# Kernel tuning notes

Measured on AMD Instinct MI355X. Metric: run time of the kernel, lower is better.

## Reference

```python
import jax, jax.numpy as jnp
import numpy as np

N_NODES = 5000
N_EDGES = 160000
HID = 64
NODE_F = 4
TASK_F = 4
BATCH = 512


def _glorot(key, shape):
    fan_in = shape[-1]
    return jax.random.normal(key, shape, dtype=jnp.float32) / jnp.sqrt(jnp.float32(fan_in))


def setup_inputs() -> dict:
    key = jax.random.key(0)
    ks = jax.random.split(key, 16)
    x = jax.random.normal(ks[0], (N_NODES, NODE_F), dtype=jnp.float32)
    edge_index = jax.random.randint(ks[1], (2, N_EDGES), 0, N_NODES, dtype=jnp.int64)
    task_feat = jax.random.normal(ks[2], (BATCH, TASK_F), dtype=jnp.float32)
    return {
        "x": x,
        "edge_index": edge_index,
        "task_feat": task_feat,
        # SAGEConv layer 1: out = lin_l(mean_neigh) + lin_r(x); lin_l has bias, lin_r (root) has no bias (PyG default)
        "Wl1": _glorot(ks[3], (HID, NODE_F)), "bl1": jnp.zeros((HID,), jnp.float32),
        "Wr1": _glorot(ks[4], (HID, NODE_F)),
        # SAGEConv layer 2
        "Wl2": _glorot(ks[5], (HID, HID)), "bl2": jnp.zeros((HID,), jnp.float32),
        "Wr2": _glorot(ks[6], (HID, HID)),
        # task_encoder: Linear(4,64) -> ReLU -> Linear(64,64)
        "Wt1": _glorot(ks[7], (HID, TASK_F)), "bt1": jnp.zeros((HID,), jnp.float32),
        "Wt2": _glorot(ks[8], (HID, HID)), "bt2": jnp.zeros((HID,), jnp.float32),
        # classifier: Linear(128,64) -> ReLU -> Linear(64,1)
        "Wc1": _glorot(ks[9], (HID, 2 * HID)), "bc1": jnp.zeros((HID,), jnp.float32),
        "Wc2": _glorot(ks[10], (1, HID)), "bc2": jnp.zeros((1,), jnp.float32),
    }


def _sage_conv(x, src, dst, Wl, bl, Wr):
    # PyG SAGEConv(mean): messages flow src -> dst; mean over incoming neighbors
    msg_sum = jax.ops.segment_sum(x[src], dst, num_segments=N_NODES)
    deg = jax.ops.segment_sum(jnp.ones((src.shape[0],), x.dtype), dst, num_segments=N_NODES)
    mean_neigh = msg_sum / jnp.maximum(deg, 1.0)[:, None]
    return mean_neigh @ Wl.T + bl + x @ Wr.T


def reference(x, edge_index, task_feat,
              Wl1, bl1, Wr1, Wl2, bl2, Wr2,
              Wt1, bt1, Wt2, bt2, Wc1, bc1, Wc2, bc2):
    src, dst = edge_index[0], edge_index[1]
    h = jax.nn.relu(_sage_conv(x, src, dst, Wl1, bl1, Wr1))        # [N, HID]
    h = jax.nn.relu(_sage_conv(h, src, dst, Wl2, bl2, Wr2))        # [N, HID]
    t = jax.nn.relu(task_feat @ Wt1.T + bt1) @ Wt2.T + bt2         # [B, HID]
    # classifier on concat([h, t]) == split Wc1 into h-part and t-part; avoids materializing the concat
    h_part = h @ Wc1[:, :HID].T                                    # [N, HID]
    t_part = t @ Wc1[:, HID:].T + bc1                              # [B, HID]
    hidden = jax.nn.relu(h_part[None, :, :] + t_part[:, None, :])  # [B, N, HID]
    scores = jnp.einsum('bnh,h->bn', hidden, Wc2[0]) + bc2[0]      # [B, N]
    return scores
```

## Files before the change

kernel.cpp:

```cpp
#include <hip/hip_runtime.h>

#define N_NODES 5000
#define N_EDGES 160000
#define HID 64
#define BATCH 512
#define NSL 64
#define EPS (N_EDGES / NSL)
#define SLOTS 12
#define NROW (NSL * SLOTS)
#define CSTRIDE 96


__global__ __launch_bounds__(256) void sort_kernel(
        const int* __restrict__ ei, const float* __restrict__ task_feat,
        const float* __restrict__ Wt1, const float* __restrict__ bt1,
        const float* __restrict__ Wt2, const float* __restrict__ bt2,
        const float* __restrict__ Wc1, const float* __restrict__ bc1,
        const float* __restrict__ Wl1, const float* __restrict__ Wr1,
        const float* __restrict__ Wl2, const float* __restrict__ Wr2,
        int* __restrict__ slots, int* __restrict__ cnt, float* __restrict__ t_part,
        float* __restrict__ Wl1T, float* __restrict__ Wr1T,
        float* __restrict__ Wl2T, float* __restrict__ Wr2T,
        float* __restrict__ Wc1hT) {
    int tid = threadIdx.x;
    int blk = blockIdx.x;
    __shared__ union SM {
        int cur[N_NODES];
        struct { float s1[4][64]; float s2[4][64]; } t;
    } sm;

    if (blk < NSL) {
        int s = blk;
        for (int i = tid; i < N_NODES; i += 256) sm.cur[i] = 0;
        __syncthreads();
        int base = s * EPS;
        for (int j = tid; j < EPS; j += 256) {
            int src = ei[base + j];
            int dst = ei[N_EDGES + base + j];
            int q = atomicAdd(&sm.cur[dst], 1);
            if (q < SLOTS) slots[dst * NROW + s * SLOTS + q] = src;
        }
        __syncthreads();
        for (int n = tid; n < N_NODES; n += 256)
            cnt[s * N_NODES + n] = min(sm.cur[n], SLOTS);
    } else if (blk < NSL + 4) {
        int w = blk - NSL;
        if (w == 0) {
            for (int idx = tid; idx < 4096; idx += 256) {
                int k = idx >> 6, h = idx & 63;
                Wl2T[idx] = Wl2[h * 64 + k];
            }
        } else if (w == 1) {
            for (int idx = tid; idx < 4096; idx += 256) {
                int k = idx >> 6, h = idx & 63;
                Wr2T[idx] = Wr2[h * 64 + k];
            }
        } else if (w == 2) {
            for (int idx = tid; idx < 4096; idx += 256) {
                int k = idx >> 6, h = idx & 63;
                Wc1hT[idx] = Wc1[h * 128 + k];
            }
        } else {
            int k = tid >> 6, h = tid & 63;
            Wl1T[tid] = Wl1[h * 4 + k];
            Wr1T[tid] = Wr1[h * 4 + k];
        }
    } else {
        int grp = tid >> 6, h = tid & 63;
        int b = (blk - (NSL + 4)) * 4 + grp;
        float4 tf = ((const float4*)task_feat)[b];
        float4 w1 = ((const float4*)Wt1)[h];
        float v = bt1[h] + tf.x * w1.x + tf.y * w1.y + tf.z * w1.z + tf.w * w1.w;
        sm.t.s1[grp][h] = fmaxf(v, 0.f);
        __syncthreads();
        const float4* w2r = (const float4*)(Wt2 + h * 64);
        const float4* s1v = (const float4*)sm.t.s1[grp];
        float v2 = bt2[h];
#pragma unroll
        for (int q = 0; q < 16; q++) {
            float4 w = w2r[q]; float4 ss = s1v[q];
            v2 += ss.x * w.x + ss.y * w.y + ss.z * w.z + ss.w * w.w;
        }
        sm.t.s2[grp][h] = v2;
        __syncthreads();
        const float4* wcr = (const float4*)(Wc1 + h * 128 + 64);
        const float4* s2v = (const float4*)sm.t.s2[grp];
        float p = bc1[h];
#pragma unroll
        for (int q = 0; q < 16; q++) {
            float4 w = wcr[q]; float4 ss = s2v[q];
            p += ss.x * w.x + ss.y * w.y + ss.z * w.z + ss.w * w.w;
        }
        t_part[b * 64 + h] = p;
    }
}

__global__ __launch_bounds__(256) void layer1_kernel(
        const float* __restrict__ x, const int* __restrict__ slots,
        const int* __restrict__ cnt,
        const float* __restrict__ Wl1T, const float* __restrict__ bl1,
        const float* __restrict__ Wr1T,
        int* __restrict__ deg, int* __restrict__ compact, float* __restrict__ h1) {
    int lane = threadIdx.x & 63, grp = threadIdx.x >> 6;
    int n = blockIdx.x * 4 + grp;
    int c = cnt[lane * N_NODES + n];
    int scan = c;
#pragma unroll
    for (int off = 1; off < 64; off <<= 1) {
        int nb = __shfl_up(scan, off);
        if (lane >= off) scan += nb;
    }
    int d = __shfl(scan, 63);
    int excl = scan - c;
    const int* chunk = slots + n * NROW + lane * SLOTS;
    float4 xs = make_float4(0.f, 0.f, 0.f, 0.f);
    for (int q = 0; q < c; q++) {
        int src = chunk[q];
        float4 xv = ((const float4*)x)[src];
        xs.x += xv.x; xs.y += xv.y; xs.z += xv.z; xs.w += xv.w;
        int pos = excl + q;
        if (pos < CSTRIDE) compact[n * CSTRIDE + pos] = src;
    }
#pragma unroll
    for (int off = 1; off < 64; off <<= 1) {
        xs.x += __shfl_xor(xs.x, off);
        xs.y += __shfl_xor(xs.y, off);
        xs.z += __shfl_xor(xs.z, off);
        xs.w += __shfl_xor(xs.w, off);
    }
    if (d > CSTRIDE) d = CSTRIDE;
    if (lane == 0) deg[n] = d;
    float inv = 1.f / fmaxf((float)d, 1.f);
    float m0 = xs.x * inv, m1 = xs.y * inv, m2 = xs.z * inv, m3 = xs.w * inv;
    float4 xn = ((const float4*)x)[n];
    float v = bl1[lane]
            + m0 * Wl1T[lane] + m1 * Wl1T[64 + lane]
            + m2 * Wl1T[128 + lane] + m3 * Wl1T[192 + lane]
            + xn.x * Wr1T[lane] + xn.y * Wr1T[64 + lane]
            + xn.z * Wr1T[128 + lane] + xn.w * Wr1T[192 + lane];
    h1[n * 64 + lane] = fmaxf(v, 0.f);
}

__global__ __launch_bounds__(256) void layer2_kernel(
        const float* __restrict__ h1, const int* __restrict__ deg,
        const int* __restrict__ compact,
        const float* __restrict__ Wl2T, const float* __restrict__ bl2,
        const float* __restrict__ Wr2T, const float* __restrict__ Wc1hT,
        float* __restrict__ h_part) {
    int h = threadIdx.x & 63, grp = threadIdx.x >> 6;
    int n = blockIdx.x * 4 + grp;
    int d = deg[n];
    const int* bucket = compact + n * CSTRIDE;
    float a0 = 0.f, a1 = 0.f, a2 = 0.f, a3 = 0.f;
    int j = 0;
    for (; j + 4 <= d; j += 4) {
        int e0 = bucket[j], e1 = bucket[j + 1], e2 = bucket[j + 2], e3 = bucket[j + 3];
        a0 += h1[e0 * 64 + h];
        a1 += h1[e1 * 64 + h];
        a2 += h1[e2 * 64 + h];
        a3 += h1[e3 * 64 + h];
    }
    for (; j < d; j++) a0 += h1[bucket[j] * 64 + h];
    float m = (a0 + a1 + a2 + a3) / fmaxf((float)d, 1.f);

    __shared__ float shm[4][64], shh[4][64], shh2[4][64];
    shm[grp][h] = m;
    shh[grp][h] = h1[n * 64 + h];
    __syncthreads();
    float v = bl2[h];
#pragma unroll
    for (int k = 0; k < 64; k++)
        v += shm[grp][k] * Wl2T[k * 64 + h] + shh[grp][k] * Wr2T[k * 64 + h];
    shh2[grp][h] = fmaxf(v, 0.f);
    __syncthreads();
    float p = 0.f;
#pragma unroll
    for (int k = 0; k < 64; k++) p += shh2[grp][k] * Wc1hT[k * 64 + h];
    h_part[n * 64 + h] = p;
}

__global__ __launch_bounds__(256) void scores_kernel(
        const float* __restrict__ h_part, const float* __restrict__ t_part,
        const float* __restrict__ Wc2, const float* __restrict__ bc2,
        float* __restrict__ out) {
    int tid = threadIdx.x;
    int n = blockIdx.x * 256 + tid;
    bool valid = n < N_NODES;
    int nn = valid ? n : (N_NODES - 1);
    float hr[64];
    const float4* hp = (const float4*)(h_part + nn * 64);
#pragma unroll
    for (int i = 0; i < 16; i++) {
        float4 v = hp[i];
        hr[4 * i + 0] = v.x; hr[4 * i + 1] = v.y;
        hr[4 * i + 2] = v.z; hr[4 * i + 3] = v.w;
    }
    float b2 = bc2[0];
    int b0 = blockIdx.y * 8;
    for (int bb = 0; bb < 8; bb++) {
        const float* tp = t_part + (b0 + bb) * 64;
        float acc = 0.f;
#pragma unroll
        for (int h = 0; h < 64; h++)
            acc = fmaf(fmaxf(hr[h] + tp[h], 0.f), Wc2[h], acc);
        if (valid) out[(b0 + bb) * N_NODES + n] = acc + b2;
    }
}

extern "C" void kernel_launch(void* const* d_in, const int* in_sizes, int n_in,
                              void* d_out, int out_size, void* d_ws, size_t ws_size,
                              hipStream_t stream) {
    const float* x    = (const float*)d_in[0];
    const int*   ei   = (const int*)d_in[1];
    const float* task = (const float*)d_in[2];
    const float* Wl1  = (const float*)d_in[3];
    const float* bl1  = (const float*)d_in[4];
    const float* Wr1  = (const float*)d_in[5];
    const float* Wl2  = (const float*)d_in[6];
    const float* bl2  = (const float*)d_in[7];
    const float* Wr2  = (const float*)d_in[8];
    const float* Wt1  = (const float*)d_in[9];
    const float* bt1  = (const float*)d_in[10];
    const float* Wt2  = (const float*)d_in[11];
    const float* bt2  = (const float*)d_in[12];
    const float* Wc1  = (const float*)d_in[13];
    const float* bc1  = (const float*)d_in[14];
    const float* Wc2  = (const float*)d_in[15];
    const float* bc2  = (const float*)d_in[16];
    float* out = (float*)d_out;

    char* ws = (char*)d_ws;
    int*   slots   = (int*)(ws + 0);
    int*   cnt     = (int*)(ws + 15360000);
    int*   compact = (int*)(ws + 16640000);
    int*   deg     = (int*)(ws + 18560000);
    float* h1      = (float*)(ws + 18580000);
    float* h_part  = (float*)(ws + 19860000);
    float* t_part  = (float*)(ws + 21140000);
    float* Wl1T  = (float*)(ws + 21271072);
    float* Wr1T  = (float*)(ws + 21272096);
    float* Wl2T  = (float*)(ws + 21273120);
    float* Wr2T  = (float*)(ws + 21289504);
    float* Wc1hT = (float*)(ws + 21305888);

    sort_kernel<<<NSL + 4 + BATCH / 4, 256, 0, stream>>>(
        ei, task, Wt1, bt1, Wt2, bt2, Wc1, bc1, Wl1, Wr1, Wl2, Wr2,
        slots, cnt, t_part, Wl1T, Wr1T, Wl2T, Wr2T, Wc1hT);
    layer1_kernel<<<N_NODES / 4, 256, 0, stream>>>(x, slots, cnt, Wl1T, bl1, Wr1T,
                                                   deg, compact, h1);
    layer2_kernel<<<N_NODES / 4, 256, 0, stream>>>(h1, deg, compact, Wl2T, bl2, Wr2T,
                                                   Wc1hT, h_part);
    scores_kernel<<<dim3(20, 64), 256, 0, stream>>>(h_part, t_part, Wc2, bc2, out);
}
```

Baseline: 148.1 us.

## Drop weight transpose pass, stage weights in LDS, reslice slot layout

Removes the global weight-transpose blocks from the sort kernel. Layer2 now loads the raw row-major weights into padded LDS tiles in every block and reads them with float4 dot products, and layer1 reads the original weight rows as float4. The slot buffer is reorganised per slice (slice-major, node, slot) so each sort block writes a contiguous region, and the scores kernel processes 16 batches per block instead of 8. The trade-off is that every layer2 block reloads about 48KB of weights into LDS, which lowers occupancy and repeats global reads.

```diff
diff --git a/kernel.cpp b/kernel.cpp
--- a/kernel.cpp
+++ b/kernel.cpp
@@ -7,7 +7,6 @@
 #define NSL 64
 #define EPS (N_EDGES / NSL)
 #define SLOTS 12
-#define NROW (NSL * SLOTS)
 #define CSTRIDE 96
 
 
@@ -16,12 +15,7 @@
         const float* __restrict__ Wt1, const float* __restrict__ bt1,
         const float* __restrict__ Wt2, const float* __restrict__ bt2,
         const float* __restrict__ Wc1, const float* __restrict__ bc1,
-        const float* __restrict__ Wl1, const float* __restrict__ Wr1,
-        const float* __restrict__ Wl2, const float* __restrict__ Wr2,
-        int* __restrict__ slots, int* __restrict__ cnt, float* __restrict__ t_part,
-        float* __restrict__ Wl1T, float* __restrict__ Wr1T,
-        float* __restrict__ Wl2T, float* __restrict__ Wr2T,
-        float* __restrict__ Wc1hT) {
+        int* __restrict__ slots, int* __restrict__ cnt, float* __restrict__ t_part) {
     int tid = threadIdx.x;
     int blk = blockIdx.x;
     __shared__ union SM {
@@ -34,40 +28,19 @@
         for (int i = tid; i < N_NODES; i += 256) sm.cur[i] = 0;
         __syncthreads();
         int base = s * EPS;
+        int* myslots = slots + s * (N_NODES * SLOTS);
         for (int j = tid; j < EPS; j += 256) {
             int src = ei[base + j];
             int dst = ei[N_EDGES + base + j];
             int q = atomicAdd(&sm.cur[dst], 1);
-            if (q < SLOTS) slots[dst * NROW + s * SLOTS + q] = src;
+            if (q < SLOTS) myslots[dst * SLOTS + q] = src;
         }
         __syncthreads();
         for (int n = tid; n < N_NODES; n += 256)
             cnt[s * N_NODES + n] = min(sm.cur[n], SLOTS);
-    } else if (blk < NSL + 4) {
-        int w = blk - NSL;
-        if (w == 0) {
-            for (int idx = tid; idx < 4096; idx += 256) {
-                int k = idx >> 6, h = idx & 63;
-                Wl2T[idx] = Wl2[h * 64 + k];
-            }
-        } else if (w == 1) {
-            for (int idx = tid; idx < 4096; idx += 256) {
-                int k = idx >> 6, h = idx & 63;
-                Wr2T[idx] = Wr2[h * 64 + k];
-            }
-        } else if (w == 2) {
-            for (int idx = tid; idx < 4096; idx += 256) {
-                int k = idx >> 6, h = idx & 63;
-                Wc1hT[idx] = Wc1[h * 128 + k];
-            }
-        } else {
-            int k = tid >> 6, h = tid & 63;
-            Wl1T[tid] = Wl1[h * 4 + k];
-            Wr1T[tid] = Wr1[h * 4 + k];
-        }
     } else {
         int grp = tid >> 6, h = tid & 63;
-        int b = (blk - (NSL + 4)) * 4 + grp;
+        int b = (blk - NSL) * 4 + grp;
         float4 tf = ((const float4*)task_feat)[b];
         float4 w1 = ((const float4*)Wt1)[h];
         float v = bt1[h] + tf.x * w1.x + tf.y * w1.y + tf.z * w1.z + tf.w * w1.w;
@@ -98,8 +71,8 @@
 __global__ __launch_bounds__(256) void layer1_kernel(
         const float* __restrict__ x, const int* __restrict__ slots,
         const int* __restrict__ cnt,
-        const float* __restrict__ Wl1T, const float* __restrict__ bl1,
-        const float* __restrict__ Wr1T,
+        const float* __restrict__ Wl1, const float* __restrict__ bl1,
+        const float* __restrict__ Wr1,
         int* __restrict__ deg, int* __restrict__ compact, float* __restrict__ h1) {
     int lane = threadIdx.x & 63, grp = threadIdx.x >> 6;
     int n = blockIdx.x * 4 + grp;
@@ -112,7 +85,7 @@
     }
     int d = __shfl(scan, 63);
     int excl = scan - c;
-    const int* chunk = slots + n * NROW + lane * SLOTS;
+    const int* chunk = slots + (lane * N_NODES + n) * SLOTS;
     float4 xs = make_float4(0.f, 0.f, 0.f, 0.f);
     for (int q = 0; q < c; q++) {
         int src = chunk[q];
@@ -131,24 +104,36 @@
     if (d > CSTRIDE) d = CSTRIDE;
     if (lane == 0) deg[n] = d;
     float inv = 1.f / fmaxf((float)d, 1.f);
-    float m0 = xs.x * inv, m1 = xs.y * inv, m2 = xs.z * inv, m3 = xs.w * inv;
     float4 xn = ((const float4*)x)[n];
+    float4 wl = ((const float4*)Wl1)[lane];
+    float4 wr = ((const float4*)Wr1)[lane];
     float v = bl1[lane]
-            + m0 * Wl1T[lane] + m1 * Wl1T[64 + lane]
-            + m2 * Wl1T[128 + lane] + m3 * Wl1T[192 + lane]
-            + xn.x * Wr1T[lane] + xn.y * Wr1T[64 + lane]
-            + xn.z * Wr1T[128 + lane] + xn.w * Wr1T[192 + lane];
+            + (xs.x * inv) * wl.x + (xs.y * inv) * wl.y
+            + (xs.z * inv) * wl.z + (xs.w * inv) * wl.w
+            + xn.x * wr.x + xn.y * wr.y + xn.z * wr.z + xn.w * wr.w;
     h1[n * 64 + lane] = fmaxf(v, 0.f);
 }
 
-__global__ __launch_bounds__(256) void layer2_kernel(
+#define WS65 65
+__global__ __launch_bounds__(256, 3) void layer2_kernel(
         const float* __restrict__ h1, const int* __restrict__ deg,
         const int* __restrict__ compact,
-        const float* __restrict__ Wl2T, const float* __restrict__ bl2,
-        const float* __restrict__ Wr2T, const float* __restrict__ Wc1hT,
+        const float* __restrict__ Wl2, const float* __restrict__ bl2,
+        const float* __restrict__ Wr2, const float* __restrict__ Wc1,
         float* __restrict__ h_part) {
-    int h = threadIdx.x & 63, grp = threadIdx.x >> 6;
+    int tid = threadIdx.x;
+    int h = tid & 63, grp = tid >> 6;
     int n = blockIdx.x * 4 + grp;
+    __shared__ float lw_l2[64 * WS65], lw_r2[64 * WS65], lw_c1[64 * WS65];
+    __shared__ float shm[4][64], shh[4][64], shh2[4][64];
+
+    for (int idx = tid; idx < 4096; idx += 256) {
+        int r = idx >> 6, c = idx & 63;
+        lw_l2[r * WS65 + c] = Wl2[idx];
+        lw_r2[r * WS65 + c] = Wr2[idx];
+        lw_c1[r * WS65 + c] = Wc1[r * 128 + c];
+    }
+
     int d = deg[n];
     const int* bucket = compact + n * CSTRIDE;
     float a0 = 0.f, a1 = 0.f, a2 = 0.f, a3 = 0.f;
@@ -163,19 +148,32 @@
     for (; j < d; j++) a0 += h1[bucket[j] * 64 + h];
     float m = (a0 + a1 + a2 + a3) / fmaxf((float)d, 1.f);
 
-    __shared__ float shm[4][64], shh[4][64], shh2[4][64];
     shm[grp][h] = m;
     shh[grp][h] = h1[n * 64 + h];
     __syncthreads();
+
+    const float4* mv = (const float4*)shm[grp];
+    const float4* hv = (const float4*)shh[grp];
+    const float4* wl = (const float4*)(lw_l2 + h * WS65);
+    const float4* wr = (const float4*)(lw_r2 + h * WS65);
     float v = bl2[h];
 #pragma unroll
-    for (int k = 0; k < 64; k++)
-        v += shm[grp][k] * Wl2T[k * 64 + h] + shh[grp][k] * Wr2T[k * 64 + h];
+    for (int q = 0; q < 16; q++) {
+        float4 a = wl[q]; float4 b = wr[q];
+        float4 mm = mv[q]; float4 hh = hv[q];
+        v += mm.x * a.x + mm.y * a.y + mm.z * a.z + mm.w * a.w
+           + hh.x * b.x + hh.y * b.y + hh.z * b.z + hh.w * b.w;
+    }
     shh2[grp][h] = fmaxf(v, 0.f);
     __syncthreads();
+    const float4* h2v = (const float4*)shh2[grp];
+    const float4* wc = (const float4*)(lw_c1 + h * WS65);
     float p = 0.f;
 #pragma unroll
-    for (int k = 0; k < 64; k++) p += shh2[grp][k] * Wc1hT[k * 64 + h];
+    for (int q = 0; q < 16; q++) {
+        float4 c = wc[q]; float4 s = h2v[q];
+        p += s.x * c.x + s.y * c.y + s.z * c.z + s.w * c.w;
+    }
     h_part[n * 64 + h] = p;
 }
 
@@ -196,8 +194,8 @@
         hr[4 * i + 2] = v.z; hr[4 * i + 3] = v.w;
     }
     float b2 = bc2[0];
-    int b0 = blockIdx.y * 8;
-    for (int bb = 0; bb < 8; bb++) {
+    int b0 = blockIdx.y * 16;
+    for (int bb = 0; bb < 16; bb++) {
         const float* tp = t_part + (b0 + bb) * 64;
         float acc = 0.f;
 #pragma unroll
@@ -237,18 +235,12 @@
     float* h1      = (float*)(ws + 18580000);
     float* h_part  = (float*)(ws + 19860000);
     float* t_part  = (float*)(ws + 21140000);
-    float* Wl1T  = (float*)(ws + 21271072);
-    float* Wr1T  = (float*)(ws + 21272096);
-    float* Wl2T  = (float*)(ws + 21273120);
-    float* Wr2T  = (float*)(ws + 21289504);
-    float* Wc1hT = (float*)(ws + 21305888);
-
-    sort_kernel<<<NSL + 4 + BATCH / 4, 256, 0, stream>>>(
-        ei, task, Wt1, bt1, Wt2, bt2, Wc1, bc1, Wl1, Wr1, Wl2, Wr2,
-        slots, cnt, t_part, Wl1T, Wr1T, Wl2T, Wr2T, Wc1hT);
-    layer1_kernel<<<N_NODES / 4, 256, 0, stream>>>(x, slots, cnt, Wl1T, bl1, Wr1T,
+
+    sort_kernel<<<NSL + BATCH / 4, 256, 0, stream>>>(
+        ei, task, Wt1, bt1, Wt2, bt2, Wc1, bc1, slots, cnt, t_part);
+    layer1_kernel<<<N_NODES / 4, 256, 0, stream>>>(x, slots, cnt, Wl1, bl1, Wr1,
                                                    deg, compact, h1);
-    layer2_kernel<<<N_NODES / 4, 256, 0, stream>>>(h1, deg, compact, Wl2T, bl2, Wr2T,
-                                                   Wc1hT, h_part);
-    scores_kernel<<<dim3(20, 64), 256, 0, stream>>>(h_part, t_part, Wc2, bc2, out);
-}
+    layer2_kernel<<<N_NODES / 4, 256, 0, stream>>>(h1, deg, compact,
+                                                   Wl2, bl2, Wr2, Wc1, h_part);
+    scores_kernel<<<dim3(20, 32), 256, 0, stream>>>(h_part, t_part, Wc2, bc2, out);
+}
```

Result: slower. 171.0 us (+15.5%).
